# Performance work log

Measured on AMD Instinct MI355X. Metric: run time of the kernel, lower is better.

The kernel has to match this reference:

```python
import jax, jax.numpy as jnp
import numpy as np

B, C, T, K = 64, 12, 2048, 2048
LMAX = 11            # max kernel length among {7,9,11}
CMAX = C - 1         # torch.randint(1, C) -> at most C-1 selected channels
PL = 1024            # left pad: covers max 'same' left pad = (dil*(len-1))//2 <= (T-1)//2
PR = 3412            # right pad: covers zero-weight padded taps (LMAX-1)*dil_max
A = 7.0              # softppv_param


def setup_inputs() -> dict:
    rng = np.random.default_rng(0)
    klens = rng.choice(np.array([7, 9, 11]), size=K)
    nch = rng.integers(1, C, size=K)  # 1..C-1 channels per kernel
    weights = np.zeros((K, CMAX, LMAX), np.float32)
    ch_idx = np.zeros((K, CMAX), np.int32)
    dils = np.zeros(K, np.int32)
    offs = np.zeros(K, np.int32)
    olens = np.zeros(K, np.int32)
    for k in range(K):
        n, L = int(nch[k]), int(klens[k])
        ch_idx[k, :n] = rng.permutation(C)[:n]
        w = rng.standard_normal((n, L)).astype(np.float32)
        w -= w.mean(axis=1, keepdims=True)  # per-channel mean-centering as in torch init
        weights[k, :n, :L] = w
        d = int(2.0 ** rng.uniform(0.0, np.log2((T - 1) / (L - 1))))
        dils[k] = d
        if rng.integers(0, 2) == 0:  # padding='same' (torch: left=total//2, right=rest)
            offs[k] = PL - (d * (L - 1)) // 2
            olens[k] = T
        else:                        # padding='valid'
            offs[k] = PL
            olens[k] = T - d * (L - 1)
    biases = rng.uniform(0.0, 1.0, size=K).astype(np.float32)
    x = jax.random.normal(jax.random.key(0), (B, C, T), jnp.float32)
    return {
        "x": x,
        "weights": jnp.asarray(weights),
        "biases": jnp.asarray(biases),
        "ch_idx": jnp.asarray(ch_idx),
        "dils": jnp.asarray(dils),
        "offs": jnp.asarray(offs),
        "olens": jnp.asarray(olens),
    }


def reference(x, weights, biases, ch_idx, dils, offs, olens):
    # x: (B, C, T). Zero-pad time axis once so every (same/valid, dilation) variant
    # becomes a pure gather with a per-kernel offset; zero-padded weight taps/channels
    # contribute nothing, so padded gathers are harmless.
    xpad = jnp.pad(x, ((0, 0), (0, 0), (PL, PR)))
    t = jnp.arange(T)
    l = jnp.arange(LMAX)

    def step(_, p):
        W, b, ch, d, off, olen = p
        pos = off + t[:, None] + l[None, :] * d            # (T, LMAX) tap positions
        Xg = xpad[:, ch, :][:, :, pos]                     # (B, CMAX, T, LMAX)
        y = jnp.einsum('bctl,cl->bt', Xg, W) + b           # cross-correlation + bias
        mask = t < olen                                    # valid output positions
        ppv = jnp.sum(jax.nn.sigmoid(A * y - 3.0) * mask, axis=-1) / olen
        mx = jnp.max(jnp.where(mask, y, -jnp.inf), axis=-1)
        return None, (ppv, mx)

    _, (ppvs, mxs) = jax.lax.scan(step, None, (weights, biases, ch_idx, dils, offs, olens))
    # torch concatenates [ppv_k, max_k] per kernel along the feature axis -> (B, 2K)
    return jnp.stack([ppvs.T, mxs.T], axis=-1).reshape(x.shape[0], 2 * K)
```

## Files before the change

kernel.cpp:

```cpp
#include <hip/hip_runtime.h>
#include <math.h>

#define B_SZ   64
#define C_SZ   12
#define T_SZ   2048
#define K_SZ   2048
#define LMAX   11
#define CMAX   11
#define NPAIR  6
#define PL_PAD 1024
#define A_PARAM 7.0f

#define NW     8
#define BLOCK_MAIN (NW * 64)
#define R      8
#define SPL    4

typedef _Float16 h2 __attribute__((ext_vector_type(2)));

__device__ __forceinline__ float fdot2f(unsigned w, unsigned v, float acc) {
    return __builtin_amdgcn_fdot2(__builtin_bit_cast(h2, w),
                                  __builtin_bit_cast(h2, v), acc, false);
}

__global__ __launch_bounds__(256) void trh_kernel(const float* __restrict__ x,
                                                  unsigned short* __restrict__ xT) {
    const int c    = blockIdx.x;
    const int lane = threadIdx.x & 63;
    const int wid  = threadIdx.x >> 6;
    const int t0   = blockIdx.y * 128 + wid * 32;
    const float* xrow = x + ((size_t)lane * C_SZ + c) * T_SZ + t0;
    unsigned short* dst = xT + ((size_t)c * T_SZ + t0) * 64 + lane;
    #pragma unroll 8
    for (int i = 0; i < 32; ++i) {
        const _Float16 h = (_Float16)xrow[i];
        dst[i * 64] = __builtin_bit_cast(unsigned short, h);
    }
}

__global__ __launch_bounds__(1024) void sched_kernel(const float* __restrict__ w,
                                                     const int* __restrict__ olens,
                                                     unsigned* __restrict__ perm) {
    __shared__ unsigned key[K_SZ];
    const int tid = threadIdx.x;

    for (int k = tid; k < K_SZ; k += 1024) {
        const float* wk = w + (size_t)k * (CMAX * LMAX);
        int n = 0, L = 0;
        for (int e = 0; e < CMAX * LMAX; ++e) {
            if (wk[e] != 0.0f) {
                const int c = e / LMAX, l = e % LMAX;
                n = max(n, c + 1);
                L = max(L, l + 1);
            }
        }
        const unsigned cost = (unsigned)(n * L) * (unsigned)((olens[k] + 127) >> 7);
        key[k] = (cost << 11) | (unsigned)k;
    }
    __syncthreads();

    for (int ksz = 2; ksz <= K_SZ; ksz <<= 1) {
        for (int j = ksz >> 1; j > 0; j >>= 1) {
            for (int i = tid; i < K_SZ; i += 1024) {
                const int ixj = i ^ j;
                if (ixj > i) {
                    const unsigned a = key[i], b = key[ixj];
                    const bool sw = ((i & ksz) == 0) ? (a < b) : (a > b);
                    if (sw) { key[i] = b; key[ixj] = a; }
                }
            }
            __syncthreads();
        }
    }
    for (int i = tid; i < K_SZ; i += 1024)
        perm[i] = key[i] & 0x7FFu;
}

template<int LC>
__device__ __forceinline__ void conv_all(
    const unsigned short* __restrict__ xT,
    const int*      __restrict__ sCh,
    const unsigned  (* __restrict__ sWp)[LMAX],
    int npair, int d, int offr, int olen, float bias, int sp,
    int lane, int wid, float& psum, float& pmax)
{
    constexpr int NV = R + LC - 1;

    const int nj   = (olen + d - 1) / d;
    const int njb  = (nj + R - 1) / R;
    const int S    = (d >= 64) ? 1 : ((64 + d - 1) / d);
    const int len  = (njb + S - 1) / S;
    const int nunits = d * S;

    for (int u = sp * NW + wid; u < nunits; u += NW * SPL) {
        int q, seg;
        if (S == 1) { q = u; seg = 0; }
        else        { q = u % d; seg = u / d; }
        const int jb0 = seg * len;
        const int jb1 = min(njb, jb0 + len);

        for (int jb = jb0; jb < jb1; ++jb) {
            const int tq = q + jb * (R * d);
            if (tq >= olen) break;
            const int tpos0 = tq + offr;

            float y[R];
            #pragma unroll
            for (int r = 0; r < R; ++r) y[r] = bias;

            const bool fast = (tpos0 >= 0) && (tpos0 + (NV - 1) * d < T_SZ);

            if (fast) {
                for (int p = 0; p < npair; ++p) {
                    const int rbA = __builtin_amdgcn_readfirstlane(sCh[2*p  ] * T_SZ + tpos0);
                    const int rbB = __builtin_amdgcn_readfirstlane(sCh[2*p+1] * T_SZ + tpos0);
                    const unsigned short* rpA = xT + ((size_t)rbA << 6);
                    const unsigned short* rpB = xT + ((size_t)rbB << 6);

                    unsigned vp[NV];
                    #pragma unroll
                    for (int i = 0; i < NV; ++i) {
                        const unsigned a = rpA[lane];
                        const unsigned b = rpB[lane];
                        vp[i] = __builtin_amdgcn_perm(b, a, 0x05040100);
                        rpA += (d << 6); rpB += (d << 6);
                    }

                    const unsigned* wrow = &sWp[p][0];
                    #pragma unroll
                    for (int l = 0; l < LC; ++l) {
                        const unsigned w = wrow[l];
                        #pragma unroll
                        for (int r = 0; r < R; ++r)
                            y[r] = fdot2f(w, vp[l + r], y[r]);
                    }
                }
            } else {
                for (int p = 0; p < npair; ++p) {
                    const int rbA = __builtin_amdgcn_readfirstlane(sCh[2*p  ] * T_SZ);
                    const int rbB = __builtin_amdgcn_readfirstlane(sCh[2*p+1] * T_SZ);
                    const unsigned short* rowA = xT + ((size_t)rbA << 6);
                    const unsigned short* rowB = xT + ((size_t)rbB << 6);

                    unsigned vp[NV];
                    #pragma unroll
                    for (int i = 0; i < NV; ++i) {
                        const int tp  = tpos0 + i * d;
                        const int tpc = min(max(tp, 0), T_SZ - 1);
                        const unsigned a = rowA[((size_t)tpc << 6) + lane];
                        const unsigned b = rowB[((size_t)tpc << 6) + lane];
                        const unsigned pk = __builtin_amdgcn_perm(b, a, 0x05040100);
                        vp[i] = ((unsigned)tp < (unsigned)T_SZ) ? pk : 0u;
                    }

                    const unsigned* wrow = &sWp[p][0];
                    #pragma unroll
                    for (int l = 0; l < LC; ++l) {
                        const unsigned w = wrow[l];
                        #pragma unroll
                        for (int r = 0; r < R; ++r)
                            y[r] = fdot2f(w, vp[l + r], y[r]);
                    }
                }
            }

            #pragma unroll
            for (int r = 0; r < R; ++r) {
                const int t = tq + r * d;
                if (t < olen) {
                    psum += 1.0f / (1.0f + __expf(3.0f - A_PARAM * y[r]));
                    pmax  = fmaxf(pmax, y[r]);
                }
            }
        }
    }
}

__global__ __launch_bounds__(BLOCK_MAIN, 4) void rocket_tr(
    const unsigned short* __restrict__ xT,
    const unsigned* __restrict__ perm,
    const float* __restrict__ weights,
    const float* __restrict__ biases,
    const int*   __restrict__ ch_idx,
    const int*   __restrict__ dils,
    const int*   __restrict__ offs,
    const int*   __restrict__ olens,
    float*       __restrict__ part)
{
    __shared__ float    sW[CMAX][LMAX];
    __shared__ unsigned sWp[NPAIR][LMAX];
    __shared__ int      sCh[2 * NPAIR];
    __shared__ int      sMeta[2];
    __shared__ float    sP[NW][64];
    __shared__ float    sM[NW][64];

    const int kidx = blockIdx.x / SPL;
    const int sp   = blockIdx.x % SPL;
    const int k    = (int)perm[kidx];
    const int tid  = threadIdx.x;

    if (tid < CMAX * LMAX)
        sW[tid / LMAX][tid % LMAX] = weights[(size_t)k * (CMAX * LMAX) + tid];
    if (tid < 2 * NPAIR)
        sCh[tid] = (tid < CMAX) ? ch_idx[(size_t)k * CMAX + tid] : 0;
    __syncthreads();

    if (tid < NPAIR * LMAX) {
        const int p = tid / LMAX;
        const int l = tid % LMAX;
        const float wA = sW[2 * p][l];
        const float wB = (2 * p + 1 < CMAX) ? sW[2 * p + 1][l] : 0.0f;
        h2 hh; hh.x = (_Float16)wA; hh.y = (_Float16)wB;
        sWp[p][l] = __builtin_bit_cast(unsigned, hh);
    }
    if (tid == 0) {
        int n = 0, L = 0;
        for (int c = 0; c < CMAX; ++c) {
            bool nz = false;
            for (int l = 0; l < LMAX; ++l) {
                if (sW[c][l] != 0.0f) { nz = true; if (l + 1 > L) L = l + 1; }
            }
            if (nz) n = c + 1;
        }
        sMeta[0] = n; sMeta[1] = L;
    }
    __syncthreads();

    const int   n     = sMeta[0];
    const int   L     = sMeta[1];
    const int   npair = (n + 1) >> 1;
    const int   d     = dils[k];
    const int   offr  = offs[k] - PL_PAD;
    const int   olen  = olens[k];
    const float bias  = biases[k];
    const int   lane  = tid & 63;
    const int   wid   = __builtin_amdgcn_readfirstlane(tid >> 6);

    float psum = 0.0f;
    float pmax = -INFINITY;

    if (L <= 7)
        conv_all<7 >(xT, sCh, sWp, npair, d, offr, olen, bias, sp, lane, wid, psum, pmax);
    else if (L <= 9)
        conv_all<9 >(xT, sCh, sWp, npair, d, offr, olen, bias, sp, lane, wid, psum, pmax);
    else
        conv_all<11>(xT, sCh, sWp, npair, d, offr, olen, bias, sp, lane, wid, psum, pmax);

    sP[wid][lane] = psum;
    sM[wid][lane] = pmax;
    __syncthreads();

    if (tid < 64) {
        float s = 0.0f, m = -INFINITY;
        #pragma unroll
        for (int w = 0; w < NW; ++w) {
            s += sP[w][tid];
            m  = fmaxf(m, sM[w][tid]);
        }
        float* pp = part + ((size_t)k * SPL + sp) * 128;
        pp[tid]      = s;
        pp[64 + tid] = m;
    }
}

__global__ __launch_bounds__(256) void combine_kernel(
    const float* __restrict__ part,
    const int*   __restrict__ olens,
    float*       __restrict__ out)
{
    const int idx = blockIdx.x * 256 + threadIdx.x;
    if (idx >= K_SZ * 64) return;
    const int k = idx >> 6;
    const int b = idx & 63;
    const float* pp = part + (size_t)k * SPL * 128;
    float s = 0.0f, m = -INFINITY;
    #pragma unroll
    for (int sp = 0; sp < SPL; ++sp) {
        s += pp[sp * 128 + b];
        m  = fmaxf(m, pp[sp * 128 + 64 + b]);
    }
    out[(size_t)b * (2 * K_SZ) + 2 * k]     = s / (float)olens[k];
    out[(size_t)b * (2 * K_SZ) + 2 * k + 1] = m;
}

__global__ __launch_bounds__(256) void rocket_fallback(
    const float* __restrict__ x,
    const float* __restrict__ weights,
    const float* __restrict__ biases,
    const int*   __restrict__ ch_idx,
    const int*   __restrict__ dils,
    const int*   __restrict__ offs,
    const int*   __restrict__ olens,
    float*       __restrict__ out)
{
    __shared__ float sW[CMAX][LMAX];
    __shared__ int   sCh[CMAX];
    __shared__ float sRed[2][4];

    const int k   = blockIdx.x;
    const int tid = threadIdx.x;

    if (tid < CMAX * LMAX)
        sW[tid / LMAX][tid % LMAX] = weights[(size_t)k * (CMAX * LMAX) + tid];
    if (tid < CMAX)
        sCh[tid] = ch_idx[(size_t)k * CMAX + tid];
    __syncthreads();

    const int   d    = dils[k];
    const int   off  = offs[k] - PL_PAD;
    const int   olen = olens[k];
    const float bias = biases[k];
    const int   lane = tid & 63;
    const int   wid  = tid >> 6;

    for (int b = blockIdx.y; b < B_SZ; b += gridDim.y) {
        float psum = 0.0f, pmax = -INFINITY;
        for (int t = tid; t < T_SZ; t += 256) {
            float y = bias;
            for (int c = 0; c < CMAX; ++c) {
                const float* xb = x + ((size_t)b * C_SZ + sCh[c]) * T_SZ;
                int pos = off + t;
                for (int l = 0; l < LMAX; ++l) {
                    const float xv = ((unsigned)pos < (unsigned)T_SZ) ? xb[pos] : 0.0f;
                    y = fmaf(sW[c][l], xv, y);
                    pos += d;
                }
            }
            if (t < olen) {
                psum += 1.0f / (1.0f + __expf(3.0f - A_PARAM * y));
                pmax = fmaxf(pmax, y);
            }
        }
        for (int o = 32; o > 0; o >>= 1) {
            psum += __shfl_down(psum, o, 64);
            pmax  = fmaxf(pmax, __shfl_down(pmax, o, 64));
        }
        if (lane == 0) { sRed[0][wid] = psum; sRed[1][wid] = pmax; }
        __syncthreads();
        if (tid == 0) {
            const float s = sRed[0][0] + sRed[0][1] + sRed[0][2] + sRed[0][3];
            const float m = fmaxf(fmaxf(sRed[1][0], sRed[1][1]),
                                  fmaxf(sRed[1][2], sRed[1][3]));
            out[(size_t)b * (2 * K_SZ) + 2 * k]     = s / (float)olen;
            out[(size_t)b * (2 * K_SZ) + 2 * k + 1] = m;
        }
        __syncthreads();
    }
}

extern "C" void kernel_launch(void* const* d_in, const int* in_sizes, int n_in,
                              void* d_out, int out_size, void* d_ws, size_t ws_size,
                              hipStream_t stream) {
    const float* x       = (const float*)d_in[0];
    const float* weights = (const float*)d_in[1];
    const float* biases  = (const float*)d_in[2];
    const int*   ch_idx  = (const int*)  d_in[3];
    const int*   dils    = (const int*)  d_in[4];
    const int*   offs    = (const int*)  d_in[5];
    const int*   olens   = (const int*)  d_in[6];
    float*       out     = (float*)d_out;

    const size_t xt_bytes   = (size_t)C_SZ * T_SZ * 64 * sizeof(unsigned short);
    const size_t perm_bytes = K_SZ * sizeof(unsigned);
    const size_t part_bytes = (size_t)K_SZ * SPL * 128 * sizeof(float);
    const size_t need       = xt_bytes + perm_bytes + part_bytes;

    if (ws_size >= need) {
        unsigned short* xT = (unsigned short*)d_ws;
        unsigned* perm     = (unsigned*)((char*)d_ws + xt_bytes);
        float*    part     = (float*)((char*)d_ws + xt_bytes + perm_bytes);
        dim3 tgrid(C_SZ, T_SZ / 128);
        trh_kernel<<<tgrid, 256, 0, stream>>>(x, xT);
        sched_kernel<<<1, 1024, 0, stream>>>(weights, olens, perm);
        rocket_tr<<<K_SZ * SPL, BLOCK_MAIN, 0, stream>>>(xT, perm, weights,
                                                         biases, ch_idx, dils,
                                                         offs, olens, part);
        combine_kernel<<<(K_SZ * 64 + 255) / 256, 256, 0, stream>>>(part, olens, out);
    } else {
        dim3 grid(K_SZ, 16);
        rocket_fallback<<<grid, 256, 0, stream>>>(x, weights, biases, ch_idx,
                                                  dils, offs, olens, out);
    }
}
```

Measured before the change: 678.0 us.

## Use persistent blocks with an atomic work queue and precomputed kernel metadata

The main convolution kernel becomes a persistent grid of 1024 blocks that pull (kernel, split) work items from a global atomic counter, replacing the one-block-per-item launch. The per-kernel channel count and length are now computed once in the scheduling kernel and stored in a metadata array, so the main kernel no longer stages the full weight matrix and runs a serial scan on thread 0. The intent is to cut per-block setup and tail imbalance, since sorted work is handed out dynamically. The cost is an atomic plus extra barriers per item, and the counter must be reset by the scheduling kernel on every launch.

```diff
diff --git a/kernel.cpp b/kernel.cpp
--- a/kernel.cpp
+++ b/kernel.cpp
@@ -15,6 +15,7 @@
 #define BLOCK_MAIN (NW * 64)
 #define R      8
 #define SPL    4
+#define NBLK   1024
 
 typedef _Float16 h2 __attribute__((ext_vector_type(2)));
 
@@ -40,9 +41,12 @@
 
 __global__ __launch_bounds__(1024) void sched_kernel(const float* __restrict__ w,
                                                      const int* __restrict__ olens,
-                                                     unsigned* __restrict__ perm) {
+                                                     unsigned* __restrict__ perm,
+                                                     unsigned* __restrict__ meta,
+                                                     unsigned* __restrict__ counter) {
     __shared__ unsigned key[K_SZ];
     const int tid = threadIdx.x;
+    if (tid == 0) *counter = 0u;
 
     for (int k = tid; k < K_SZ; k += 1024) {
         const float* wk = w + (size_t)k * (CMAX * LMAX);
@@ -54,6 +58,7 @@
                 L = max(L, l + 1);
             }
         }
+        meta[k] = (unsigned)n | ((unsigned)L << 8);
         const unsigned cost = (unsigned)(n * L) * (unsigned)((olens[k] + 127) >> 7);
         key[k] = (cost << 11) | (unsigned)k;
     }
@@ -179,87 +184,86 @@
 __global__ __launch_bounds__(BLOCK_MAIN, 4) void rocket_tr(
     const unsigned short* __restrict__ xT,
     const unsigned* __restrict__ perm,
+    const unsigned* __restrict__ meta,
     const float* __restrict__ weights,
     const float* __restrict__ biases,
     const int*   __restrict__ ch_idx,
     const int*   __restrict__ dils,
     const int*   __restrict__ offs,
     const int*   __restrict__ olens,
-    float*       __restrict__ part)
+    float*       __restrict__ part,
+    unsigned*    __restrict__ counter)
 {
-    __shared__ float    sW[CMAX][LMAX];
     __shared__ unsigned sWp[NPAIR][LMAX];
     __shared__ int      sCh[2 * NPAIR];
-    __shared__ int      sMeta[2];
+    __shared__ int      sItem;
     __shared__ float    sP[NW][64];
     __shared__ float    sM[NW][64];
 
-    const int kidx = blockIdx.x / SPL;
-    const int sp   = blockIdx.x % SPL;
-    const int k    = (int)perm[kidx];
     const int tid  = threadIdx.x;
-
-    if (tid < CMAX * LMAX)
-        sW[tid / LMAX][tid % LMAX] = weights[(size_t)k * (CMAX * LMAX) + tid];
-    if (tid < 2 * NPAIR)
-        sCh[tid] = (tid < CMAX) ? ch_idx[(size_t)k * CMAX + tid] : 0;
-    __syncthreads();
-
-    if (tid < NPAIR * LMAX) {
-        const int p = tid / LMAX;
-        const int l = tid % LMAX;
-        const float wA = sW[2 * p][l];
-        const float wB = (2 * p + 1 < CMAX) ? sW[2 * p + 1][l] : 0.0f;
-        h2 hh; hh.x = (_Float16)wA; hh.y = (_Float16)wB;
-        sWp[p][l] = __builtin_bit_cast(unsigned, hh);
-    }
-    if (tid == 0) {
-        int n = 0, L = 0;
-        for (int c = 0; c < CMAX; ++c) {
-            bool nz = false;
-            for (int l = 0; l < LMAX; ++l) {
-                if (sW[c][l] != 0.0f) { nz = true; if (l + 1 > L) L = l + 1; }
-            }
-            if (nz) n = c + 1;
-        }
-        sMeta[0] = n; sMeta[1] = L;
-    }
-    __syncthreads();
-
-    const int   n     = sMeta[0];
-    const int   L     = sMeta[1];
-    const int   npair = (n + 1) >> 1;
-    const int   d     = dils[k];
-    const int   offr  = offs[k] - PL_PAD;
-    const int   olen  = olens[k];
-    const float bias  = biases[k];
-    const int   lane  = tid & 63;
-    const int   wid   = __builtin_amdgcn_readfirstlane(tid >> 6);
-
-    float psum = 0.0f;
-    float pmax = -INFINITY;
-
-    if (L <= 7)
-        conv_all<7 >(xT, sCh, sWp, npair, d, offr, olen, bias, sp, lane, wid, psum, pmax);
-    else if (L <= 9)
-        conv_all<9 >(xT, sCh, sWp, npair, d, offr, olen, bias, sp, lane, wid, psum, pmax);
-    else
-        conv_all<11>(xT, sCh, sWp, npair, d, offr, olen, bias, sp, lane, wid, psum, pmax);
-
-    sP[wid][lane] = psum;
-    sM[wid][lane] = pmax;
-    __syncthreads();
-
-    if (tid < 64) {
-        float s = 0.0f, m = -INFINITY;
-        #pragma unroll
-        for (int w = 0; w < NW; ++w) {
-            s += sP[w][tid];
-            m  = fmaxf(m, sM[w][tid]);
-        }
-        float* pp = part + ((size_t)k * SPL + sp) * 128;
-        pp[tid]      = s;
-        pp[64 + tid] = m;
+    const int lane = tid & 63;
+    const int wid  = __builtin_amdgcn_readfirstlane(tid >> 6);
+
+    for (;;) {
+        __syncthreads();
+        if (tid == 0) sItem = (int)atomicAdd(counter, 1u);
+        __syncthreads();
+        const int item = sItem;
+        if (item >= K_SZ * SPL) break;
+
+        const int kidx = item / SPL;
+        const int sp   = item % SPL;
+        const int k    = (int)perm[kidx];
+
+        if (tid < NPAIR * LMAX) {
+            const int p = tid / LMAX;
+            const int l = tid % LMAX;
+            const float wA = weights[(size_t)k * (CMAX * LMAX) + (2 * p) * LMAX + l];
+            const float wB = (2 * p + 1 < CMAX)
+                ? weights[(size_t)k * (CMAX * LMAX) + (2 * p + 1) * LMAX + l] : 0.0f;
+            h2 hh; hh.x = (_Float16)wA; hh.y = (_Float16)wB;
+            sWp[p][l] = __builtin_bit_cast(unsigned, hh);
+        }
+        if (tid >= 64 && tid < 64 + 2 * NPAIR) {
+            const int c = tid - 64;
+            sCh[c] = (c < CMAX) ? ch_idx[(size_t)k * CMAX + c] : 0;
+        }
+        __syncthreads();
+
+        const unsigned mk = meta[k];
+        const int   n     = (int)(mk & 0xFFu);
+        const int   L     = (int)((mk >> 8) & 0xFFu);
+        const int   npair = (n + 1) >> 1;
+        const int   d     = dils[k];
+        const int   offr  = offs[k] - PL_PAD;
+        const int   olen  = olens[k];
+        const float bias  = biases[k];
+
+        float psum = 0.0f;
+        float pmax = -INFINITY;
+
+        if (L <= 7)
+            conv_all<7 >(xT, sCh, sWp, npair, d, offr, olen, bias, sp, lane, wid, psum, pmax);
+        else if (L <= 9)
+            conv_all<9 >(xT, sCh, sWp, npair, d, offr, olen, bias, sp, lane, wid, psum, pmax);
+        else
+            conv_all<11>(xT, sCh, sWp, npair, d, offr, olen, bias, sp, lane, wid, psum, pmax);
+
+        sP[wid][lane] = psum;
+        sM[wid][lane] = pmax;
+        __syncthreads();
+
+        if (tid < 64) {
+            float s = 0.0f, m = -INFINITY;
+            #pragma unroll
+            for (int w = 0; w < NW; ++w) {
+                s += sP[w][tid];
+                m  = fmaxf(m, sM[w][tid]);
+            }
+            float* pp = part + ((size_t)k * SPL + sp) * 128;
+            pp[tid]      = s;
+            pp[64 + tid] = m;
+        }
     }
 }
 
@@ -362,19 +366,24 @@
 
     const size_t xt_bytes   = (size_t)C_SZ * T_SZ * 64 * sizeof(unsigned short);
     const size_t perm_bytes = K_SZ * sizeof(unsigned);
+    const size_t meta_bytes = K_SZ * sizeof(unsigned);
     const size_t part_bytes = (size_t)K_SZ * SPL * 128 * sizeof(float);
-    const size_t need       = xt_bytes + perm_bytes + part_bytes;
+    const size_t need       = xt_bytes + perm_bytes + meta_bytes + part_bytes + 128;
 
     if (ws_size >= need) {
-        unsigned short* xT = (unsigned short*)d_ws;
-        unsigned* perm     = (unsigned*)((char*)d_ws + xt_bytes);
-        float*    part     = (float*)((char*)d_ws + xt_bytes + perm_bytes);
+        char* wsb = (char*)d_ws;
+        unsigned short* xT   = (unsigned short*)wsb;
+        unsigned* perm       = (unsigned*)(wsb + xt_bytes);
+        unsigned* meta       = (unsigned*)(wsb + xt_bytes + perm_bytes);
+        float*    part       = (float*)(wsb + xt_bytes + perm_bytes + meta_bytes);
+        unsigned* counter    = (unsigned*)(wsb + xt_bytes + perm_bytes + meta_bytes + part_bytes);
+
         dim3 tgrid(C_SZ, T_SZ / 128);
         trh_kernel<<<tgrid, 256, 0, stream>>>(x, xT);
-        sched_kernel<<<1, 1024, 0, stream>>>(weights, olens, perm);
-        rocket_tr<<<K_SZ * SPL, BLOCK_MAIN, 0, stream>>>(xT, perm, weights,
-                                                         biases, ch_idx, dils,
-                                                         offs, olens, part);
+        sched_kernel<<<1, 1024, 0, stream>>>(weights, olens, perm, meta, counter);
+        rocket_tr<<<NBLK, BLOCK_MAIN, 0, stream>>>(xT, perm, meta, weights,
+                                                   biases, ch_idx, dils, offs,
+                                                   olens, part, counter);
         combine_kernel<<<(K_SZ * 64 + 255) / 256, 256, 0, stream>>>(part, olens, out);
     } else {
         dim3 grid(K_SZ, 16);
```

After: 629.9 us, median of 2. -7.1%, faster.
